# Optimization experiments

Hardware: AMD Instinct MI355X
Metric: run time of the kernel (lower is better)

Reference implementation:

```python
import jax, jax.numpy as jnp
import numpy as np

B, N, M, K = 2, 4096, 512, 50
EMB, OUT = 512, 128
EPS = 1e-5


def _sqdist(a, b):
    # a: [B,P,D], b: [B,Q,D] -> squared euclidean distances [B,P,Q]
    return (jnp.sum(a * a, -1)[:, :, None] + jnp.sum(b * b, -1)[:, None, :]
            - 2.0 * jnp.einsum('bpd,bqd->bpq', a, b))


def _graph_feature(x, xg, k):
    # x: [B,D,N] points, xg: [B,D,M] grid -> edge features [B,2D,N,k]
    xt = x.transpose(0, 2, 1)   # [B,N,D]
    gt = xg.transpose(0, 2, 1)  # [B,M,D]
    nearest = jnp.argmin(_sqdist(xt, gt), axis=-1)               # [B,N] nearest grid pt per point
    _, nbr = jax.lax.top_k(-_sqdist(gt, gt), k)                  # [B,M,k] kNN within grid
    idx = jnp.take_along_axis(nbr, nearest[:, :, None], axis=1)  # [B,N,k]
    b = x.shape[0]
    feat = gt[jnp.arange(b)[:, None, None], idx]                 # [B,N,k,D] gathered grid feats
    feat = feat.at[:, :, 0, :].set(xt)                           # slot 0 <- point's own feature
    ctr = xt[:, :, None, :]
    out = jnp.concatenate([feat - ctr, jnp.broadcast_to(ctr, feat.shape)], axis=-1)
    return out.transpose(0, 3, 1, 2)                             # [B,2D,N,k]


def _lrelu(x):
    return jnp.where(x >= 0, x, 0.2 * x)


def _bn(y, g, bt, axes):
    # BatchNorm forward with batch statistics (torch training-mode math, biased var)
    m = jnp.mean(y, axis=axes, keepdims=True)
    v = jnp.mean((y - m) ** 2, axis=axes, keepdims=True)
    sh = [1] * y.ndim
    sh[1] = -1
    return (y - m) / jnp.sqrt(v + EPS) * g.reshape(sh) + bt.reshape(sh)


def _conv2(x, W, g, bt):
    # 1x1 Conv2d (no bias) + BN2d + LeakyReLU(0.2)
    return _lrelu(_bn(jnp.einsum('oc,bcnk->bonk', W, x), g, bt, (0, 2, 3)))


def _conv1(x, W, g, bt):
    # 1x1 Conv1d (no bias) + BN1d + LeakyReLU(0.2)
    return _lrelu(_bn(jnp.einsum('oc,bcn->bon', W, x), g, bt, (0, 2)))


def _forward(x, x_grid, FPS, W1, W2, W3, W4, W5, W6, W7, W8, W9,
             g1, g2, g3, g4, g5, g6, g7, g8,
             b1, b2, b3, b4, b5, b6, b7, b8):
    f = _graph_feature(x, x_grid, K)
    f = _conv2(f, W1, g1, b1)
    f = _conv2(f, W2, g2, b2)
    x1 = f.max(-1)                                               # [B,64,N]
    x1g = jnp.take_along_axis(x1, FPS[:, None, :], axis=2)       # [B,64,M]
    f = _graph_feature(x1, x1g, K)
    f = _conv2(f, W3, g3, b3)
    f = _conv2(f, W4, g4, b4)
    x2 = f.max(-1)
    x2g = jnp.take_along_axis(x2, FPS[:, None, :], axis=2)
    f = _graph_feature(x2, x2g, K)
    f = _conv2(f, W5, g5, b5)
    x3 = f.max(-1)
    x3g = jnp.take_along_axis(x3, FPS[:, None, :], axis=2)
    xg = jnp.concatenate([x1g, x2g, x3g], axis=1)                # [B,192,M]
    xg = _conv1(xg, W6, g6, b6)                                  # [B,EMB,M]
    xg = jnp.broadcast_to(xg.max(-1, keepdims=True), (x.shape[0], EMB, x.shape[2]))
    h = jnp.concatenate([xg, x1, x2, x3], axis=1)                # [B,EMB+192,N]
    h = _conv1(h, W7, g7, b7)
    h = _conv1(h, W8, g8, b8)
    h = jnp.einsum('oc,bcn->bon', W9, h)                         # final conv9, no BN/act
    return h.transpose(0, 2, 1)                                  # [B,N,OUT]


def setup_inputs() -> dict:
    key = jax.random.key(0)
    ks = jax.random.split(key, 32)
    def w(i, o, c):
        return jax.random.normal(ks[i], (o, c), jnp.float32) * 0.1
    inp = {
        'x': jax.random.normal(ks[0], (B, 3, N), jnp.float32),
        'x_grid': jax.random.normal(ks[1], (B, 3, M), jnp.float32),
        'FPS': jax.random.randint(ks[2], (B, M), 0, N),
        'W1': w(3, 64, 6), 'W2': w(4, 64, 64), 'W3': w(5, 64, 128),
        'W4': w(6, 64, 64), 'W5': w(7, 64, 128), 'W6': w(8, EMB, 192),
        'W7': w(9, 128, 192 + EMB), 'W8': w(10, 64, 128), 'W9': w(11, OUT, 64),
    }
    dims = [64, 64, 64, 64, 64, EMB, 128, 64]
    for j, d in enumerate(dims):
        inp[f'g{j+1}'] = 1.0 + 0.05 * jax.random.normal(ks[12 + j], (d,), jnp.float32)
        inp[f'b{j+1}'] = 0.05 * jax.random.normal(ks[20 + j], (d,), jnp.float32)
    return inp


def reference(x, x_grid, FPS, W1, W2, W3, W4, W5, W6, W7, W8, W9,
              g1, g2, g3, g4, g5, g6, g7, g8,
              b1, b2, b3, b4, b5, b6, b7, b8):
    return _forward(x, x_grid, FPS, W1, W2, W3, W4, W5, W6, W7, W8, W9,
                    g1, g2, g3, g4, g5, g6, g7, g8,
                    b1, b2, b3, b4, b5, b6, b7, b8)
```

## Files before the change

kernel.cpp:

```cpp
#include <hip/hip_runtime.h>
#include <hip/hip_bf16.h>

#define DEV __device__ __forceinline__
using bf16 = __hip_bfloat16;
using u16 = unsigned short;
using u64 = unsigned long long;

static constexpr int B_ = 2, N_ = 4096, M_ = 512, K_ = 50;
static constexpr int BN = B_ * N_;
static constexpr int BM = B_ * M_;
static constexpr float EPS_ = 1e-5f;

DEV float lrelu(float z) { return z < 0.f ? 0.2f * z : z; }
DEV int clampi(int v, int hi) { return ((unsigned)v < (unsigned)hi) ? v : 0; }

DEV u16 f2bfu(float f) {
    unsigned u = __float_as_uint(f);
    return (u16)((u + 0x7fffu + ((u >> 16) & 1u)) >> 16);
}
DEV float bfu2f(u16 h) { return __uint_as_float((unsigned)h << 16); }
DEV unsigned cvtpk(float a, float b) {
    unsigned r;
    asm("v_cvt_pk_bf16_f32 %0, %1, %2" : "=v"(r) : "v"(a), "v"(b));
    return r;
}

typedef short bf8v __attribute__((ext_vector_type(8)));
typedef float f4v __attribute__((ext_vector_type(4)));

__global__ void k_detect(const unsigned short* __restrict__ xw, int* __restrict__ flag) {
    int t = threadIdx.x;
    int cnt = 0;
    for (int i = t; i < 4096; i += 256) {
        int e = (xw[i] >> 7) & 0xFF;
        if (e >= 100 && e <= 140) cnt++;
    }
    __shared__ int sh[256];
    sh[t] = cnt;
    __syncthreads();
    for (int s = 128; s; s >>= 1) { if (t < s) sh[t] += sh[t + s]; __syncthreads(); }
    if (t == 0) *flag = (sh[0] >= 3300) ? 1 : 0;
}

struct CvtDesc { const void* src; float* dst; int n; };
struct CvtArgs { CvtDesc d[25]; };
__global__ void k_convert(CvtArgs a, const int* __restrict__ flag) {
    CvtDesc dd = a.d[blockIdx.y];
    int i = blockIdx.x * 256 + threadIdx.x;
    if (i >= dd.n) return;
    float v = (*flag) ? __bfloat162float(((const bf16*)dd.src)[i])
                      : ((const float*)dd.src)[i];
    dd.dst[i] = v;
}

struct CvtT { const void* src; float* dst; int O; int C; int stride; int off; };
struct CvtTArgs { CvtT d[6]; };
__global__ void k_convT(CvtTArgs a, const int* __restrict__ flag) {
    CvtT dd = a.d[blockIdx.y];
    int idx = blockIdx.x * 256 + threadIdx.x;
    if (idx >= dd.O * dd.C) return;
    int c = idx / dd.O, o = idx % dd.O;
    int si = o * dd.stride + dd.off + c;
    float v = (*flag) ? __bfloat162float(((const bf16*)dd.src)[si])
                      : ((const float*)dd.src)[si];
    dd.dst[idx] = v;
}

__global__ void k_wfrag(const float* __restrict__ Wa, const float* __restrict__ Wb,
                        u16* __restrict__ fa, u16* __restrict__ fb) {
    const float* W = blockIdx.y ? Wb : Wa;
    u16* f = blockIdx.y ? fb : fa;
    int t = blockIdx.x * 256 + threadIdx.x;
    int j = t & 7, l = (t >> 3) & 63, s = (t >> 9) & 1, n = (t >> 10) & 3;
    int o = n * 16 + (l & 15);
    int c = s * 32 + (l >> 4) * 8 + j;
    float v = W[o * 64 + c];
    u16 hi = f2bfu(v);
    u16 lo = f2bfu(v - bfu2f(hi));
    f[t] = hi;
    f[4096 + t] = lo;
}

__global__ void k_wfrag7(const float* __restrict__ W7vt, u16* __restrict__ f) {
    int t = blockIdx.x * 256 + threadIdx.x;
    int j = t & 7, l = (t >> 3) & 63;
    int rest = t >> 9;
    int s = rest % 6, ot = rest / 6;
    int o = ot * 16 + (l & 15);
    int c = s * 32 + (l >> 4) * 8 + j;
    float v = W7vt[c * 128 + o];
    u16 hi = f2bfu(v);
    u16 lo = f2bfu(v - bfu2f(hi));
    f[t] = hi;
    f[24576 + t] = lo;
}

__global__ void k_ubuf(const float* __restrict__ Pg, const float* __restrict__ prm,
                       float* __restrict__ ub) {
    int t = blockIdx.x * 256 + threadIdx.x;
    int c = t & 63;
    ub[t] = fmaf(prm[c], Pg[t], prm[64 + c]);
}

DEV float rdval(const void* p, int i, int isbf) {
    return isbf ? __bfloat162float(((const bf16*)p)[i]) : ((const float*)p)[i];
}
__global__ void k_transpose(const void* __restrict__ x, const void* __restrict__ xg,
                            const int* __restrict__ flag,
                            float* __restrict__ xt, float* __restrict__ gt,
                            float* __restrict__ gT3, float* __restrict__ gn) {
    int isbf = *flag;
    int idx = blockIdx.x * 256 + threadIdx.x;
    if (idx < BN * 3) {
        int c = idx / BN, i = idx % BN;
        int b = i / N_, n = i % N_;
        xt[i * 3 + c] = rdval(x, (b * 3 + c) * N_ + n, isbf);
    } else {
        int r = idx - BN * 3;
        if (r < BM) {
            int b = r / M_, m = r % M_;
            float s = 0.f;
            for (int c = 0; c < 3; c++) {
                float v = rdval(xg, (b * 3 + c) * M_ + m, isbf);
                gt[r * 3 + c] = v;
                gT3[(b * 3 + c) * M_ + m] = v;
                s = fmaf(v, v, s);
            }
            gn[r] = s;
        }
    }
}

DEV void nearest3_body(int blk, const float* __restrict__ q, const float* __restrict__ gt,
                       const float* __restrict__ gn, int* __restrict__ nearest) {
    int sub = threadIdx.x & 15;
    int pt = blk * 16 + (threadIdx.x >> 4);
    int b = pt >> 12;
    float q0 = q[pt * 3], q1 = q[pt * 3 + 1], q2 = q[pt * 3 + 2];
    float qn = q0 * q0 + q1 * q1 + q2 * q2;
    const float* gb = gt + (size_t)b * M_ * 3;
    const float* gnb = gn + b * M_;
    float best = 1e30f; int bi = 0x7fffffff;
    for (int j = 0; j < 32; j++) {
        int m = sub + 16 * j;
        float dot = q0 * gb[m * 3] + q1 * gb[m * 3 + 1] + q2 * gb[m * 3 + 2];
        float dv = qn + gnb[m] - 2.f * dot;
        if (dv < best || (dv == best && m < bi)) { best = dv; bi = m; }
    }
    for (int off = 8; off; off >>= 1) {
        float ov = __shfl_xor(best, off);
        int oi = __shfl_xor(bi, off);
        if (ov < best || (ov == best && oi < bi)) { best = ov; bi = oi; }
    }
    if (sub == 0) nearest[pt] = clampi(bi, M_);
}

DEV void nearest64_body_v4(int blk, const float* __restrict__ q,
                           const float* __restrict__ gT, const float* __restrict__ gn,
                           int* __restrict__ nearest,
                           float (*__restrict__ lg)[512], float (*__restrict__ ql)[64]) {
    int lane = threadIdx.x & 63;
    int tid = threadIdx.x;
    int w = __builtin_amdgcn_readfirstlane(threadIdx.x >> 6);
    int pt0 = blk * 16 + w * 4;
    int b = pt0 >> 12;
    const float* gTb = gT + (size_t)b * 64 * M_;
    {
        const float4* q4 = (const float4*)(q + (size_t)(blk * 16) * 64);
        ((float4*)ql)[tid] = q4[tid];
    }
    float qn[4] = {0.f, 0.f, 0.f, 0.f};
    float d[4][8] = {};
#pragma clang loop unroll(disable)
    for (int ch = 0; ch < 8; ch++) {
        __syncthreads();
        {
            const float4* src = (const float4*)(gTb + (size_t)ch * 8 * M_);
            float4* dst = (float4*)lg;
#pragma unroll
            for (int i = 0; i < 4; i++) {
                int idx = i * 256 + tid;
                dst[idx] = src[idx];
            }
        }
        __syncthreads();
#pragma unroll
        for (int j = 0; j < 8; j++) {
            float4 g0 = *(const float4*)&lg[j][4 * lane];
            float4 g1 = *(const float4*)&lg[j][256 + 4 * lane];
#pragma unroll
            for (int p = 0; p < 4; p++) {
                float qc = ql[w * 4 + p][ch * 8 + j];
                qn[p] = fmaf(qc, qc, qn[p]);
                d[p][0] = fmaf(qc, g0.x, d[p][0]); d[p][1] = fmaf(qc, g0.y, d[p][1]);
                d[p][2] = fmaf(qc, g0.z, d[p][2]); d[p][3] = fmaf(qc, g0.w, d[p][3]);
                d[p][4] = fmaf(qc, g1.x, d[p][4]); d[p][5] = fmaf(qc, g1.y, d[p][5]);
                d[p][6] = fmaf(qc, g1.z, d[p][6]); d[p][7] = fmaf(qc, g1.w, d[p][7]);
            }
        }
    }
    const float* gnb = gn + b * M_;
    float4 n0 = *(const float4*)(gnb + 4 * lane);
    float4 n1 = *(const float4*)(gnb + 256 + 4 * lane);
    float nn[8] = {n0.x, n0.y, n0.z, n0.w, n1.x, n1.y, n1.z, n1.w};
#pragma clang loop unroll(disable)
    for (int p = 0; p < 4; p++) {
        float best = 1e30f; int bi = 0;
#pragma unroll
        for (int i = 0; i < 8; i++) {
            int m = (i < 4) ? (4 * lane + i) : (256 + 4 * lane + i - 4);
            float dv = qn[p] + nn[i] - 2.f * d[p][i];
            if (dv < best || (dv == best && m < bi)) { best = dv; bi = m; }
        }
        for (int off = 32; off; off >>= 1) {
            float ov = __shfl_xor(best, off);
            int oi = __shfl_xor(bi, off);
            if (ov < best || (ov == best && oi < bi)) { best = ov; bi = oi; }
        }
        if (lane == 0) nearest[pt0 + p] = clampi(bi, M_);
    }
}

DEV void select50(const float dd[8], const int mreg[8], int lane,
                  int* __restrict__ rowp, int* __restrict__ idxrow) {
    u64 key[8];
#pragma unroll
    for (int i = 0; i < 8; i++) {
        unsigned u = __float_as_uint(dd[i]);
        if (u == 0x80000000u) u = 0u;
        u = (u & 0x80000000u) ? ~u : (u | 0x80000000u);
        key[i] = ((u64)u << 9) | (u64)(unsigned)mreg[i];
    }
    u64 kmin = key[0];
#pragma unroll
    for (int i = 1; i < 8; i++) kmin = key[i] < kmin ? key[i] : kmin;
    for (int off = 32; off; off >>= 1) {
        u64 o = __shfl_xor(kmin, off);
        kmin = o < kmin ? o : kmin;
    }
    u64 res = 0;
#pragma clang loop unroll(disable)
    for (int bit = 40; bit >= 0; --bit) {
        u64 t = res | ((u64)1 << bit);
        int c = 0;
#pragma unroll
        for (int i = 0; i < 8; i++) c += (key[i] < t) ? 1 : 0;
        u64 b0 = __ballot(c & 1), b1 = __ballot(c & 2), b2 = __ballot(c & 4), b3 = __ballot(c & 8);
        int tot = __popcll(b0) + 2 * __popcll(b1) + 4 * __popcll(b2) + 8 * __popcll(b3);
        if (tot <= K_ - 1) res = t;
    }
    int lc = 0, loc[8];
    bool sel[8];
#pragma unroll
    for (int i = 0; i < 8; i++) {
        sel[i] = (key[i] <= res) && (key[i] != kmin);
        loc[i] = lc;
        lc += sel[i] ? 1 : 0;
    }
    u64 lmask = ((u64)1 << lane) - 1;
    u64 c0 = __ballot(lc & 1), c1 = __ballot(lc & 2), c2 = __ballot(lc & 4), c3 = __ballot(lc & 8);
    int pre = __popcll(c0 & lmask) + 2 * __popcll(c1 & lmask)
            + 4 * __popcll(c2 & lmask) + 8 * __popcll(c3 & lmask);
#pragma unroll
    for (int i = 0; i < 8; i++) {
        if (key[i] == kmin) { rowp[0] = mreg[i]; idxrow[0] = mreg[i]; }
        if (sel[i]) { int p = 1 + pre + loc[i]; rowp[p] = mreg[i]; idxrow[p] = mreg[i]; }
    }
}

DEV void nbr3_body(int blk, const float* __restrict__ g, const float* __restrict__ gT,
                   const float* __restrict__ gn, const float* __restrict__ Pg,
                   int* __restrict__ nbr, float* __restrict__ T1, float* __restrict__ T2,
                   float* __restrict__ Mn, float* __restrict__ Mx,
                   int (*__restrict__ idxb)[64]) {
    int lane = threadIdx.x & 63, w = threadIdx.x >> 6;
    int row = blk * 4 + w;
    int b = row >> 9;
    const float* grow = g + (size_t)row * 3;
    float qn = gn[row];
    const float* gTb = gT + (size_t)b * 3 * M_;
    const float* gnb = gn + b * M_;
// ... 73 lines not shown
        for (int j = 0; j < 8; j++) {
            float qc = ql[w][ch * 8 + j];
            float4 g0 = *(const float4*)&lg[j][4 * lane];
            float4 g1 = *(const float4*)&lg[j][256 + 4 * lane];
            d[0] = fmaf(qc, g0.x, d[0]); d[1] = fmaf(qc, g0.y, d[1]);
            d[2] = fmaf(qc, g0.z, d[2]); d[3] = fmaf(qc, g0.w, d[3]);
            d[4] = fmaf(qc, g1.x, d[4]); d[5] = fmaf(qc, g1.y, d[5]);
            d[6] = fmaf(qc, g1.z, d[6]); d[7] = fmaf(qc, g1.w, d[7]);
        }
    }
    float4 n0 = *(const float4*)(gnb + 4 * lane);
    float4 n1 = *(const float4*)(gnb + 256 + 4 * lane);
    float dd[8];
    dd[0] = qn + n0.x - 2.f * d[0]; dd[1] = qn + n0.y - 2.f * d[1];
    dd[2] = qn + n0.z - 2.f * d[2]; dd[3] = qn + n0.w - 2.f * d[3];
    dd[4] = qn + n1.x - 2.f * d[4]; dd[5] = qn + n1.y - 2.f * d[5];
    dd[6] = qn + n1.z - 2.f * d[6]; dd[7] = qn + n1.w - 2.f * d[7];
    int mreg[8];
#pragma unroll
    for (int i = 0; i < 8; i++) mreg[i] = (i < 4) ? (4 * lane + i) : (256 + 4 * lane + i - 4);
    select50(dd, mreg, lane, nbr + (size_t)row * K_, idxb[w]);
    int myIdx = idxb[w][lane];
    const float* Pgb = Pg + (size_t)b * M_ * 64;
    float t1 = 0.f, t2 = 0.f, mn = 1e30f, mx = -1e30f;
#pragma unroll 7
    for (int k = 1; k < K_; k++) {
        int idx = clampi(__shfl(myIdx, k), M_);
        float v = Pgb[(size_t)idx * 64 + lane];
        t1 += v; t2 = fmaf(v, v, t2);
        mn = fminf(mn, v); mx = fmaxf(mx, v);
    }
    size_t o = (size_t)row * 64 + lane;
    T1[o] = t1; T2[o] = t2; Mn[o] = mn; Mx[o] = mx;
}

__global__ __launch_bounds__(256) void k_knn3(
    const float* __restrict__ q, const float* __restrict__ gt, const float* __restrict__ gT3,
    const float* __restrict__ gn, const float* __restrict__ Pg,
    int* __restrict__ nearest, int* __restrict__ nbr, float* __restrict__ T1,
    float* __restrict__ T2, float* __restrict__ Mn, float* __restrict__ Mx) {
    __shared__ int idxb[4][64];
    if (blockIdx.x < BN / 16) nearest3_body(blockIdx.x, q, gt, gn, nearest);
    else nbr3_body(blockIdx.x - BN / 16, gt, gT3, gn, Pg, nbr, T1, T2, Mn, Mx, idxb);
}
__global__ __launch_bounds__(256) void k_knn64(
    const float* __restrict__ q, const float* __restrict__ xgt, const float* __restrict__ gT,
    const float* __restrict__ gn, const float* __restrict__ Pg,
    int* __restrict__ nearest, int* __restrict__ nbr, float* __restrict__ T1,
    float* __restrict__ T2, float* __restrict__ Mn, float* __restrict__ Mx) {
    __shared__ float lg[8][512];
    __shared__ float ql[16][64];
    __shared__ int idxb[4][64];
    if (blockIdx.x < BN / 16) nearest64_body_v4(blockIdx.x, q, gT, gn, nearest, lg, ql);
    else nbr64_body(blockIdx.x - BN / 16, xgt, gT, gn, Pg, nbr, T1, T2, Mn, Mx, lg, ql, idxb);
}

#define STATS_STORE_64(s1v, s2v, partial)                                         \
    {                                                                             \
        __shared__ float r1_[256], r2_[256];                                      \
        r1_[threadIdx.x] = (s1v); r2_[threadIdx.x] = (s2v);                       \
        __syncthreads();                                                          \
        if (threadIdx.x < 64) {                                                   \
            int t_ = threadIdx.x;                                                 \
            float a1_ = r1_[t_] + r1_[t_ + 64] + r1_[t_ + 128] + r1_[t_ + 192];   \
            float a2_ = r2_[t_] + r2_[t_ + 64] + r2_[t_ + 128] + r2_[t_ + 192];   \
            float* sp_ = (partial) + (size_t)blockIdx.x * 128;                    \
            sp_[t_] = a1_; sp_[64 + t_] = a2_;                                    \
        }                                                                         \
    }

__global__ __launch_bounds__(256) void k_pgrid3(const float* __restrict__ g,
                                                const float* __restrict__ W1,
                                                float* __restrict__ Pg) {
    int lane = threadIdx.x & 63;
    int row = blockIdx.x * 4 + __builtin_amdgcn_readfirstlane(threadIdx.x >> 6);
    float c0 = g[row * 3], c1 = g[row * 3 + 1], c2 = g[row * 3 + 2];
    const float* wr = W1 + lane * 6;
    Pg[(size_t)row * 64 + lane] = fmaf(wr[0], c0, fmaf(wr[1], c1, wr[2] * c2));
}

__global__ __launch_bounds__(256) void k_gridprep(
    const float* __restrict__ xsrc, const int* __restrict__ FPS,
    const float* __restrict__ Wt, float* __restrict__ xgt, float* __restrict__ gT,
    float* __restrict__ gn, float* __restrict__ Pg) {
    int lane = threadIdx.x & 63, w = threadIdx.x >> 6;
    int row = blockIdx.x * 4 + w;
    int b = row >> 9, m = row & 511;
    int src = b * N_ + clampi(FPS[row], N_);
    float ge = xsrc[(size_t)src * 64 + lane];
    xgt[(size_t)row * 64 + lane] = ge;
    gT[((size_t)b * 64 + lane) * M_ + m] = ge;
    float s = 0.f, acc = 0.f;
#pragma unroll
    for (int c = 0; c < 64; c++) {
        float vc = __shfl(ge, c);
        s = fmaf(vc, vc, s);
        acc = fmaf(Wt[c * 64 + lane], vc, acc);
    }
    Pg[(size_t)row * 64 + lane] = acc;
    if (lane == 0) gn[row] = s;
}

template <int D>
__global__ __launch_bounds__(256) void k_prep_stats(
    const float* __restrict__ q, const float* __restrict__ W1,
    const int* __restrict__ nearest, const float* __restrict__ T1,
    const float* __restrict__ T2, float* __restrict__ D0, float* __restrict__ S0,
    float* __restrict__ partial) {
    int lane = threadIdx.x & 63;
    int pt = blockIdx.x * 4 + __builtin_amdgcn_readfirstlane(threadIdx.x >> 6);
    int b = pt >> 12;
    float pa, pb;
    if constexpr (D == 3) {
        float c0 = q[pt * 3], c1 = q[pt * 3 + 1], c2 = q[pt * 3 + 2];
        const float* wr = W1 + lane * 6;
        pa = fmaf(wr[0], c0, fmaf(wr[1], c1, wr[2] * c2));
        pb = fmaf(wr[3], c0, fmaf(wr[4], c1, wr[5] * c2));
    } else {
        float ge = q[(size_t)pt * 64 + lane];
        pa = 0.f; pb = 0.f;
#pragma unroll
        for (int c = 0; c < 64; c++) {
            float sh = __shfl(ge, c);
            pa = fmaf(W1[c * 64 + lane], sh, pa);
            pb = fmaf(W1[(64 + c) * 64 + lane], sh, pb);
        }
    }
    float d0 = pb - pa, s0 = pb;
    size_t t = (size_t)pt * 64 + lane;
    D0[t] = d0;
    S0[t] = s0;
    size_t nr = ((size_t)b * M_ + clampi(nearest[pt], M_)) * 64 + lane;
    float t1 = T1[nr], t2 = T2[nr];
    float s1 = s0 + fmaf(49.f, d0, t1);
    float s2 = fmaf(s0, s0, fmaf(49.f * d0, d0, fmaf(2.f * d0, t1, t2)));
    STATS_STORE_64(s1, s2, partial)
}

__global__ void k_apply0(const float* __restrict__ D0, const float* __restrict__ S0,
                         const int* __restrict__ nearest, const float* __restrict__ Mn,
                         const float* __restrict__ Mx, const float* __restrict__ prm,
                         float* __restrict__ xout) {
    int t = blockIdx.x * 256 + threadIdx.x;
    int pt = t >> 6, o = t & 63;
    int b = pt >> 12;
    size_t nr = ((size_t)b * M_ + clampi(nearest[pt], M_)) * 64 + o;
    float d0 = D0[t], s0 = S0[t];
    float a = prm[o], sh = prm[64 + o];
    float v = a > 0.f ? fmaxf(s0, d0 + Mx[nr]) : fminf(s0, d0 + Mn[nr]);
    xout[t] = lrelu(fmaf(a, v, sh));
}

__global__ __launch_bounds__(256) void k_pass1_mfma(
    const float* __restrict__ ub, const float* __restrict__ D0,
    const float* __restrict__ S0, const int* __restrict__ nearest,
    const int* __restrict__ nbr, const float* __restrict__ prm1,
    const u16* __restrict__ wf, float* __restrict__ partial,
    float* __restrict__ mn_out, float* __restrict__ mx_out) {
    __shared__ u16 Zs[2][2][4096];
    __shared__ int idxl[2][64];
    float* ls1 = (float*)&Zs[0][0][0];
    float* ls2 = ls1 + 128;
    int l = threadIdx.x & 63;
    int w = threadIdx.x >> 6;
    int wp = w >> 1, nh = w & 1;
    bf8v whi[2][2], wlo[2][2];
#pragma unroll
    for (int nt = 0; nt < 2; nt++)
#pragma unroll
        for (int s = 0; s < 2; s++) {
            int fi = (((nh * 2 + nt) * 2 + s) * 64 + l) * 8;
            whi[nt][s] = *(const bf8v*)(wf + fi);
            wlo[nt][s] = *(const bf8v*)(wf + 4096 + fi);
        }
    if (threadIdx.x < 128) {
        int p2 = threadIdx.x >> 6, k = threadIdx.x & 63;
        int pt2 = blockIdx.x * 2 + p2, b2 = pt2 >> 12;
        int nr = clampi(nearest[pt2], M_);
        idxl[p2][k] = (k >= 1 && k < K_)
                          ? clampi(nbr[((size_t)b2 * M_ + nr) * K_ + k], M_) : 0;
    }
    __syncthreads();
    {
        int tt = threadIdx.x & 127;
        int p = threadIdx.x >> 7;
        int pt = blockIdx.x * 2 + p, b = pt >> 12;
        int g = tt >> 4, j = tt & 15;
        char* zh = (char*)&Zs[p][0][0];
        char* zl = (char*)&Zs[p][1][0];
        float4 a = ((const float4*)prm1)[j];
        float4 sh4 = ((const float4*)(prm1 + 64))[j];
        float4 dv = ((const float4*)(D0 + (size_t)pt * 64))[j];
        const float* ubb = ub + (size_t)b * M_ * 64;
#pragma unroll
        for (int s = 0; s < 8; s++) {
            int k = s * 8 + g;
            float4 u, d = dv;
            if (k == 0) {
                float4 s0 = ((const float4*)(S0 + (size_t)pt * 64))[j];
                u.x = fmaf(a.x, s0.x, sh4.x); u.y = fmaf(a.y, s0.y, sh4.y);
                u.z = fmaf(a.z, s0.z, sh4.z); u.w = fmaf(a.w, s0.w, sh4.w);
                d.x = 0.f; d.y = 0.f; d.z = 0.f; d.w = 0.f;
            } else {
                int idx = idxl[p][k];
                u = ((const float4*)(ubb + (size_t)idx * 64))[j];
            }
            float z0 = lrelu(fmaf(a.x, d.x, u.x));
            float z1 = lrelu(fmaf(a.y, d.y, u.y));
            float z2 = lrelu(fmaf(a.z, d.z, u.z));
            float z3 = lrelu(fmaf(a.w, d.w, u.w));
            if (k >= K_) { z0 = 0.f; z1 = 0.f; z2 = 0.f; z3 = 0.f; }
            unsigned h01 = cvtpk(z0, z1), h23 = cvtpk(z2, z3);
            float r0 = z0 - __uint_as_float(h01 << 16);
            float r1 = z1 - __uint_as_float(h01 & 0xFFFF0000u);
            float r2 = z2 - __uint_as_float(h23 << 16);
            float r3 = z3 - __uint_as_float(h23 & 0xFFFF0000u);
            unsigned l01 = cvtpk(r0, r1), l23 = cvtpk(r2, r3);
            int ad = k * 128 + ((j * 8) ^ ((k & 7) << 4));
            *(uint2*)(zh + ad) = make_uint2(h01, h23);
            *(uint2*)(zl + ad) = make_uint2(l01, l23);
        }
    }
    __syncthreads();
    int pt = blockIdx.x * 2 + wp;
    const char* zh = (const char*)&Zs[wp][0][0];
    const char* zl = (const char*)&Zs[wp][1][0];
    f4v acc[4][2] = {};
#pragma unroll
    for (int s = 0; s < 2; s++) {
        bf8v ah[4], al[4];
#pragma unroll
        for (int m = 0; m < 4; m++) {
            int row = m * 16 + (l & 15);
            int ad = row * 128 + (((s * 64) + ((l >> 4) * 16)) ^ ((row & 7) << 4));
            ah[m] = *(const bf8v*)(zh + ad);
            al[m] = *(const bf8v*)(zl + ad);
        }
#pragma unroll
        for (int m = 0; m < 4; m++)
#pragma unroll
            for (int nt = 0; nt < 2; nt++) {
                acc[m][nt] = __builtin_amdgcn_mfma_f32_16x16x32_bf16(ah[m], whi[nt][s], acc[m][nt], 0, 0, 0);
                acc[m][nt] = __builtin_amdgcn_mfma_f32_16x16x32_bf16(al[m], whi[nt][s], acc[m][nt], 0, 0, 0);
                acc[m][nt] = __builtin_amdgcn_mfma_f32_16x16x32_bf16(ah[m], wlo[nt][s], acc[m][nt], 0, 0, 0);
            }
    }
    __syncthreads();
    int rg = (l >> 4) * 4;
#pragma unroll
    for (int nt = 0; nt < 2; nt++) {
        float s1 = 0.f, s2 = 0.f, mn = 1e30f, mx = -1e30f;
#pragma unroll
        for (int m = 0; m < 4; m++)
#pragma unroll
            for (int i = 0; i < 4; i++) {
                int kk = m * 16 + rg + i;
                float v = acc[m][nt][i];
                if (kk < K_) { s1 += v; s2 = fmaf(v, v, s2); mn = fminf(mn, v); mx = fmaxf(mx, v); }
            }
        for (int off = 16; off <= 32; off <<= 1) {
            s1 += __shfl_xor(s1, off); s2 += __shfl_xor(s2, off);
            mn = fminf(mn, __shfl_xor(mn, off)); mx = fmaxf(mx, __shfl_xor(mx, off));
        }
        if (l < 16) {
            int o = nh * 32 + nt * 16 + l;
            mn_out[(size_t)pt * 64 + o] = mn;
            mx_out[(size_t)pt * 64 + o] = mx;
            ls1[wp * 64 + o] = s1;
            ls2[wp * 64 + o] = s2;
        }
    }
    __syncthreads();
    if (threadIdx.x < 64) {
        int t = threadIdx.x;
        float* sp = partial + (size_t)blockIdx.x * 128;
        sp[t] = ls1[t] + ls1[64 + t];
        sp[64 + t] = ls2[t] + ls2[64 + t];
    }
}

__global__ void k_apply(const float* __restrict__ mn, const float* __restrict__ mx,
                        const float* __restrict__ prm, float* __restrict__ xout) {
    int t = blockIdx.x * 256 + threadIdx.x;
    int o = t & 63;
    float a = prm[o], sh = prm[64 + o];
    float v = a > 0.f ? mx[t] : mn[t];
    xout[t] = lrelu(fmaf(a, v, sh));
}

template <int NP, int O>
__global__ __launch_bounds__(256) void k_redfin(
    const float* __restrict__ partial, double* __restrict__ red,
    int* __restrict__ counter, int C,
    const float* __restrict__ g, const float* __restrict__ bt,
    float* __restrict__ prm) {
    constexpr int VALS = 2 * O;
    constexpr int G = NP / 32;
    int b = blockIdx.x;
    for (int v = threadIdx.x; v < VALS; v += 256) {
        const float* p = partial + (size_t)b * G * VALS + v;
        double s = 0.0;
        for (int k = 0; k < G; k++) s += p[(size_t)k * VALS];
        red[(size_t)b * VALS + v] = s;
    }
    __threadfence();
    __syncthreads();
    __shared__ bool isLast;
    if (threadIdx.x == 0) isLast = (atomicAdd(counter, 1) == 31);
    __syncthreads();
    if (!isLast) return;
    __threadfence();
    for (int o = threadIdx.x; o < O; o += 256) {
        double s1 = 0.0, s2 = 0.0;
#pragma unroll
        for (int k = 0; k < 32; k++) {
            s1 += red[(size_t)k * VALS + o];
            s2 += red[(size_t)k * VALS + O + o];
        }
        double m = s1 / C, var = s2 / C - m * m;
        if (var < 0) var = 0;
        float sc = g[o] / sqrtf((float)var + EPS_);
        prm[o] = sc;
        prm[O + o] = bt[o] - (float)m * sc;
    }
}

__global__ __launch_bounds__(256) void k_conv_w6(
    const float* __restrict__ x1gt, const float* __restrict__ x2gt,
    const float* __restrict__ x3t, const int* __restrict__ FPS,
    const float* __restrict__ W6t, float* __restrict__ y6, float* __restrict__ partial) {
    __shared__ float vl[4][192];
    int b = blockIdx.x / 128;
    int m0 = (blockIdx.x % 128) * 4;
    for (int i = threadIdx.x; i < 4 * 192; i += 256) {
        int mi = i / 192, c = i % 192;
        float v;
        if (c < 128) {
            const float* src = c < 64 ? x1gt : x2gt;
            v = src[((size_t)b * M_ + m0 + mi) * 64 + (c & 63)];
        } else {
            int s = b * N_ + clampi(FPS[b * M_ + m0 + mi], N_);
            v = x3t[(size_t)s * 64 + (c - 128)];
        }
        vl[mi][c] = v;
    }
    __syncthreads();
    float acc0[4] = {0}, acc1[4] = {0};
    int o0 = threadIdx.x, o1 = threadIdx.x + 256;
    for (int c = 0; c < 192; c++) {
        float w0 = W6t[c * 512 + o0];
        float w1 = W6t[c * 512 + o1];
#pragma unroll
        for (int m = 0; m < 4; m++) { float v = vl[m][c]; acc0[m] = fmaf(w0, v, acc0[m]); acc1[m] = fmaf(w1, v, acc1[m]); }
    }
    float s1a = 0, s2a = 0, s1b = 0, s2b = 0;
    for (int m = 0; m < 4; m++) {
        float ya = acc0[m], yb = acc1[m];
        y6[((size_t)b * M_ + m0 + m) * 512 + o0] = ya;
// ... 70 lines not shown
            else sp_ = x3t + base + (seg - 8) * 16;
            float f[16];
#pragma unroll
            for (int i = 0; i < 4; i++) {
                float4 v = ((const float4*)sp_)[i];
                f[4 * i] = v.x; f[4 * i + 1] = v.y; f[4 * i + 2] = v.z; f[4 * i + 3] = v.w;
            }
            unsigned hp[8], lp[8];
#pragma unroll
            for (int e = 0; e < 8; e++) {
                unsigned h = cvtpk(f[2 * e], f[2 * e + 1]);
                float r0 = f[2 * e] - __uint_as_float(h << 16);
                float r1 = f[2 * e + 1] - __uint_as_float(h & 0xFFFF0000u);
                hp[e] = h;
                lp[e] = cvtpk(r0, r1);
            }
            uint4* dh = (uint4*)&Zh[item][seg * 16];
            uint4* dl = (uint4*)&Zl[item][seg * 16];
            dh[0] = make_uint4(hp[0], hp[1], hp[2], hp[3]);
            dh[1] = make_uint4(hp[4], hp[5], hp[6], hp[7]);
            dl[0] = make_uint4(lp[0], lp[1], lp[2], lp[3]);
            dl[1] = make_uint4(lp[4], lp[5], lp[6], lp[7]);
        }
    }
    __syncthreads();
    f4v acc[2] = {};
#pragma unroll
    for (int s = 0; s < 6; s++) {
        int row = l & 15, col = s * 32 + (l >> 4) * 8;
        bf8v ah = *(const bf8v*)&Zh[row][col];
        bf8v al = *(const bf8v*)&Zl[row][col];
#pragma unroll
        for (int nt = 0; nt < 2; nt++) {
            acc[nt] = __builtin_amdgcn_mfma_f32_16x16x32_bf16(ah, wh[nt][s], acc[nt], 0, 0, 0);
            acc[nt] = __builtin_amdgcn_mfma_f32_16x16x32_bf16(al, wh[nt][s], acc[nt], 0, 0, 0);
            acc[nt] = __builtin_amdgcn_mfma_f32_16x16x32_bf16(ah, wl[nt][s], acc[nt], 0, 0, 0);
        }
    }
#pragma unroll
    for (int nt = 0; nt < 2; nt++) {
        int o = (2 * w + nt) * 16 + (l & 15);
        float pv = p7[b * 128 + o];
        float s1 = 0.f, s2 = 0.f;
#pragma unroll
        for (int i = 0; i < 4; i++) {
            int item = (l >> 4) * 4 + i;
            float yv = pv + acc[nt][i];
            y7[(size_t)(item0 + item) * 128 + o] = yv;
            s1 += yv; s2 = fmaf(yv, yv, s2);
        }
        for (int off = 16; off <= 32; off <<= 1) {
            s1 += __shfl_xor(s1, off);
            s2 += __shfl_xor(s2, off);
        }
        if (l < 16) {
            float* sp = partial + (size_t)blockIdx.x * 256;
            sp[o] = s1;
            sp[128 + o] = s2;
        }
    }
}

__global__ __launch_bounds__(256) void k_conv_w8(
    const float* __restrict__ y7, const float* __restrict__ prm7,
    const float* __restrict__ W8t, float* __restrict__ y8, float* __restrict__ partial) {
    int lane = threadIdx.x & 63;
    int item = blockIdx.x * 4 + (threadIdx.x >> 6);
    float W0[64], W1r[64];
#pragma unroll
    for (int c = 0; c < 64; c++) {
        W0[c] = W8t[c * 64 + lane];
        W1r[c] = W8t[(64 + c) * 64 + lane];
    }
    float a0 = prm7[lane], sh0 = prm7[128 + lane];
    float a1 = prm7[64 + lane], sh1 = prm7[128 + 64 + lane];
    float z0 = lrelu(fmaf(a0, y7[(size_t)item * 128 + lane], sh0));
    float z1 = lrelu(fmaf(a1, y7[(size_t)item * 128 + 64 + lane], sh1));
    float acc = 0.f;
#pragma unroll
    for (int c = 0; c < 64; c++) {
        acc = fmaf(W0[c], __shfl(z0, c), acc);
        acc = fmaf(W1r[c], __shfl(z1, c), acc);
    }
    y8[(size_t)item * 64 + lane] = acc;
    STATS_STORE_64(acc, acc * acc, partial)
}

__global__ __launch_bounds__(256) void k_final(
    const float* __restrict__ y8, const float* __restrict__ prm8,
    const float* __restrict__ W9t, void* __restrict__ out, const int* __restrict__ flag) {
    __shared__ float zl[2][64];
    int item0 = blockIdx.x * 2;
    if (threadIdx.x < 128) {
        int it = threadIdx.x >> 6, c = threadIdx.x & 63;
        float z = fmaf(prm8[c], y8[(size_t)(item0 + it) * 64 + c], prm8[64 + c]);
        zl[it][c] = lrelu(z);
    }
    __syncthreads();
    int it = threadIdx.x >> 7, o = threadIdx.x & 127;
    float acc = 0.f;
#pragma unroll
    for (int c = 0; c < 64; c++) acc = fmaf(W9t[c * 128 + o], zl[it][c], acc);
    size_t oi = (size_t)(item0 + it) * 128 + o;
    if (*flag) ((bf16*)out)[oi] = __float2bfloat16(acc);
    else ((float*)out)[oi] = acc;
}

extern "C" void kernel_launch(void* const* d_in, const int* in_sizes, int n_in,
                              void* d_out, int out_size, void* d_ws, size_t ws_size,
                              hipStream_t stream) {
    (void)in_sizes; (void)n_in; (void)out_size; (void)ws_size;
    const void* x = d_in[0];
    const void* xgrid = d_in[1];
    const int* FPS = (const int*)d_in[2];

    char* ws = (char*)d_ws;
    size_t off = 0;
    auto alloc = [&](size_t bytes) -> char* {
        char* p = ws + off;
        off = (off + bytes + 255) & ~(size_t)255;
        return p;
    };
    int* flag       = (int*)alloc(256);
    int* counters   = (int*)alloc(256);
    float* partials = (float*)alloc((size_t)4096 * 128 * sizeof(float));
    double* redbuf  = (double*)alloc(32 * 1024 * sizeof(double));
    float* prm      = (float*)alloc(8 * 1024 * sizeof(float));
    static const int wsz[9] = {384, 4096, 8192, 4096, 8192, 98304, 90112, 8192, 8192};
    static const int dims[8] = {64, 64, 64, 64, 64, 512, 128, 64};
    float* cW[9];
    for (int i = 0; i < 9; i++) cW[i] = (float*)alloc((size_t)wsz[i] * 4);
    float* cG[8];
    float* cB[8];
    for (int j = 0; j < 8; j++) {
        cG[j] = (float*)alloc((size_t)dims[j] * 4);
        cB[j] = (float*)alloc((size_t)dims[j] * 4);
    }
    float* W6t  = (float*)alloc((size_t)512 * 192 * 4);
    float* W7vt = (float*)alloc((size_t)128 * 192 * 4);
    float* W8t  = (float*)alloc((size_t)64 * 128 * 4);
    float* W9t  = (float*)alloc((size_t)128 * 64 * 4);
    float* W3t  = (float*)alloc((size_t)64 * 128 * 4);
    float* W5t  = (float*)alloc((size_t)64 * 128 * 4);
    u16* wf2    = (u16*)alloc((size_t)8192 * 2);
    u16* wf4    = (u16*)alloc((size_t)8192 * 2);
    u16* wf7    = (u16*)alloc((size_t)49152 * 2);
    float* xt    = (float*)alloc((size_t)BN * 3 * 4);
    float* gt    = (float*)alloc((size_t)BM * 3 * 4);
    float* gT3   = (float*)alloc((size_t)B_ * 3 * M_ * 4);
    float* gn    = (float*)alloc((size_t)BM * 4);
    int* nearest = (int*)alloc((size_t)BN * 4);
    int* nbr     = (int*)alloc((size_t)BM * K_ * 4);
    float* Pg    = (float*)alloc((size_t)BM * 64 * 4);
    float* ubuf  = (float*)alloc((size_t)BM * 64 * 4);
    float* x1t   = (float*)alloc((size_t)BN * 64 * 4);
    float* x2t   = (float*)alloc((size_t)BN * 64 * 4);
    float* x3t   = (float*)alloc((size_t)BN * 64 * 4);
    float* x1gt  = (float*)alloc((size_t)BM * 64 * 4);
    float* x2gt  = (float*)alloc((size_t)BM * 64 * 4);
    float* gT64  = (float*)alloc((size_t)B_ * 64 * M_ * 4);
    float* y6    = (float*)alloc((size_t)BM * 512 * 4);
    float* xgmax = (float*)alloc((size_t)B_ * 512 * 4);
    float* p7    = (float*)alloc((size_t)B_ * 128 * 4);
    float* y7    = (float*)alloc((size_t)BN * 128 * 4);
    float* y8    = (float*)alloc((size_t)BN * 64 * 4);
    float* D0b = y7;
    float* S0b = y7 + (size_t)BN * 64;
    float* mnb = y8;
    float* mxb = y6;
    float* T1b = y6;
    float* T2b = y6 + (size_t)BM * 64;
    float* Mnb = y6 + (size_t)2 * BM * 64;
    float* Mxb = y6 + (size_t)3 * BM * 64;

    hipMemsetAsync(counters, 0, 8 * sizeof(int), stream);
    k_detect<<<1, 256, 0, stream>>>((const unsigned short*)x, flag);

    CvtArgs ca;
    for (int i = 0; i < 9; i++) ca.d[i] = {d_in[3 + i], cW[i], wsz[i]};
    for (int j = 0; j < 8; j++) {
        ca.d[9 + 2 * j]     = {d_in[12 + 2 * j], cG[j], dims[j]};
        ca.d[9 + 2 * j + 1] = {d_in[13 + 2 * j], cB[j], dims[j]};
    }
    k_convert<<<dim3(384, 25), 256, 0, stream>>>(ca, flag);
    CvtTArgs ct;
    ct.d[0] = {d_in[8],  W6t,  512, 192, 192, 0};
    ct.d[1] = {d_in[9],  W7vt, 128, 192, 704, 512};
    ct.d[2] = {d_in[10], W8t,  64, 128, 128, 0};
    ct.d[3] = {d_in[11], W9t,  128, 64, 64, 0};
    ct.d[4] = {d_in[5],  W3t,  64, 128, 128, 0};
    ct.d[5] = {d_in[7],  W5t,  64, 128, 128, 0};
    k_convT<<<dim3(384, 6), 256, 0, stream>>>(ct, flag);
    k_wfrag<<<dim3(16, 2), 256, 0, stream>>>(cW[1], cW[3], wf2, wf4);
    k_wfrag7<<<96, 256, 0, stream>>>(W7vt, wf7);
    k_transpose<<<(BN * 3 + BM + 255) / 256, 256, 0, stream>>>(x, xgrid, flag, xt, gt, gT3, gn);

    const int PG = BN / 4;
    const int EW = BN * 64 / 256;
    const int CK = BN * K_;
    const int KNNG = BN / 16 + BM / 4;
    const int UBG = BM * 64 / 256;

    k_pgrid3<<<BM / 4, 256, 0, stream>>>(gt, cW[0], Pg);
    k_knn3<<<KNNG, 256, 0, stream>>>(xt, gt, gT3, gn, Pg, nearest, nbr, T1b, T2b, Mnb, Mxb);
    k_prep_stats<3><<<PG, 256, 0, stream>>>(xt, cW[0], nearest, T1b, T2b, D0b, S0b, partials);
    k_redfin<2048, 64><<<32, 256, 0, stream>>>(partials, redbuf, counters + 0, CK, cG[0], cB[0], prm + 0 * 1024);
    k_ubuf<<<UBG, 256, 0, stream>>>(Pg, prm + 0 * 1024, ubuf);
    k_pass1_mfma<<<BN / 2, 256, 0, stream>>>(ubuf, D0b, S0b, nearest, nbr, prm + 0 * 1024, wf2, partials, mnb, mxb);
    k_redfin<4096, 64><<<32, 256, 0, stream>>>(partials, redbuf, counters + 1, CK, cG[1], cB[1], prm + 1 * 1024);
    k_apply<<<EW, 256, 0, stream>>>(mnb, mxb, prm + 1 * 1024, x1t);

    k_gridprep<<<BM / 4, 256, 0, stream>>>(x1t, FPS, W3t, x1gt, gT64, gn, Pg);
    k_knn64<<<KNNG, 256, 0, stream>>>(x1t, x1gt, gT64, gn, Pg, nearest, nbr, T1b, T2b, Mnb, Mxb);
    k_prep_stats<64><<<PG, 256, 0, stream>>>(x1t, W3t, nearest, T1b, T2b, D0b, S0b, partials);
    k_redfin<2048, 64><<<32, 256, 0, stream>>>(partials, redbuf, counters + 2, CK, cG[2], cB[2], prm + 2 * 1024);
    k_ubuf<<<UBG, 256, 0, stream>>>(Pg, prm + 2 * 1024, ubuf);
    k_pass1_mfma<<<BN / 2, 256, 0, stream>>>(ubuf, D0b, S0b, nearest, nbr, prm + 2 * 1024, wf4, partials, mnb, mxb);
    k_redfin<4096, 64><<<32, 256, 0, stream>>>(partials, redbuf, counters + 3, CK, cG[3], cB[3], prm + 3 * 1024);
    k_apply<<<EW, 256, 0, stream>>>(mnb, mxb, prm + 3 * 1024, x2t);

    k_gridprep<<<BM / 4, 256, 0, stream>>>(x2t, FPS, W5t, x2gt, gT64, gn, Pg);
    k_knn64<<<KNNG, 256, 0, stream>>>(x2t, x2gt, gT64, gn, Pg, nearest, nbr, T1b, T2b, Mnb, Mxb);
    k_prep_stats<64><<<PG, 256, 0, stream>>>(x2t, W5t, nearest, T1b, T2b, D0b, S0b, partials);
    k_redfin<2048, 64><<<32, 256, 0, stream>>>(partials, redbuf, counters + 4, CK, cG[4], cB[4], prm + 4 * 1024);
    k_apply0<<<EW, 256, 0, stream>>>(D0b, S0b, nearest, Mnb, Mxb, prm + 4 * 1024, x3t);

    k_conv_w6<<<BM / 4, 256, 0, stream>>>(x1gt, x2gt, x3t, FPS, W6t, y6, partials);
    k_redfin<256, 512><<<32, 256, 0, stream>>>(partials, redbuf, counters + 5, BM, cG[5], cB[5], prm + 5 * 1024);
    k_maxM<<<B_ * 64, 256, 0, stream>>>(y6, prm + 5 * 1024, xgmax);
    k_p7<<<64, 256, 0, stream>>>(xgmax, cW[6], p7);
    k_conv_w7m<<<BN / 16, 256, 0, stream>>>(x1t, x2t, x3t, p7, wf7, y7, partials);
    k_redfin<512, 128><<<32, 256, 0, stream>>>(partials, redbuf, counters + 6, BN, cG[6], cB[6], prm + 6 * 1024);
    k_conv_w8<<<BN / 4, 256, 0, stream>>>(y7, prm + 6 * 1024, W8t, y8, partials);
    k_redfin<2048, 64><<<32, 256, 0, stream>>>(partials, redbuf, counters + 7, BN, cG[7], cB[7], prm + 7 * 1024);
    k_final<<<BN / 2, 256, 0, stream>>>(y8, prm + 7 * 1024, W9t, d_out, flag);
}
```

Measured before the change: 391.9 us.

## Merge setup conversion kernels into one launch and fold ubuf into pass1

```diff
diff --git a/kernel.cpp b/kernel.cpp
--- a/kernel.cpp
+++ b/kernel.cpp
@@ -42,91 +42,77 @@
     if (t == 0) *flag = (sh[0] >= 3300) ? 1 : 0;
 }
 
+DEV float rdval(const void* p, size_t i, int isbf) {
+    return isbf ? __bfloat162float(((const bf16*)p)[i]) : ((const float*)p)[i];
+}
+
 struct CvtDesc { const void* src; float* dst; int n; };
-struct CvtArgs { CvtDesc d[25]; };
-__global__ void k_convert(CvtArgs a, const int* __restrict__ flag) {
-    CvtDesc dd = a.d[blockIdx.y];
-    int i = blockIdx.x * 256 + threadIdx.x;
-    if (i >= dd.n) return;
-    float v = (*flag) ? __bfloat162float(((const bf16*)dd.src)[i])
-                      : ((const float*)dd.src)[i];
-    dd.dst[i] = v;
-}
-
 struct CvtT { const void* src; float* dst; int O; int C; int stride; int off; };
-struct CvtTArgs { CvtT d[6]; };
-__global__ void k_convT(CvtTArgs a, const int* __restrict__ flag) {
-    CvtT dd = a.d[blockIdx.y];
-    int idx = blockIdx.x * 256 + threadIdx.x;
-    if (idx >= dd.O * dd.C) return;
-    int c = idx / dd.O, o = idx % dd.O;
-    int si = o * dd.stride + dd.off + c;
-    float v = (*flag) ? __bfloat162float(((const bf16*)dd.src)[si])
-                      : ((const float*)dd.src)[si];
-    dd.dst[idx] = v;
-}
-
-__global__ void k_wfrag(const float* __restrict__ Wa, const float* __restrict__ Wb,
-                        u16* __restrict__ fa, u16* __restrict__ fb) {
-    const float* W = blockIdx.y ? Wb : Wa;
-    u16* f = blockIdx.y ? fb : fa;
-    int t = blockIdx.x * 256 + threadIdx.x;
-    int j = t & 7, l = (t >> 3) & 63, s = (t >> 9) & 1, n = (t >> 10) & 3;
-    int o = n * 16 + (l & 15);
-    int c = s * 32 + (l >> 4) * 8 + j;
-    float v = W[o * 64 + c];
-    u16 hi = f2bfu(v);
-    u16 lo = f2bfu(v - bfu2f(hi));
-    f[t] = hi;
-    f[4096 + t] = lo;
-}
-
-__global__ void k_wfrag7(const float* __restrict__ W7vt, u16* __restrict__ f) {
-    int t = blockIdx.x * 256 + threadIdx.x;
-    int j = t & 7, l = (t >> 3) & 63;
-    int rest = t >> 9;
-    int s = rest % 6, ot = rest / 6;
-    int o = ot * 16 + (l & 15);
-    int c = s * 32 + (l >> 4) * 8 + j;
-    float v = W7vt[c * 128 + o];
-    u16 hi = f2bfu(v);
-    u16 lo = f2bfu(v - bfu2f(hi));
-    f[t] = hi;
-    f[24576 + t] = lo;
-}
-
-__global__ void k_ubuf(const float* __restrict__ Pg, const float* __restrict__ prm,
-                       float* __restrict__ ub) {
-    int t = blockIdx.x * 256 + threadIdx.x;
-    int c = t & 63;
-    ub[t] = fmaf(prm[c], Pg[t], prm[64 + c]);
-}
-
-DEV float rdval(const void* p, int i, int isbf) {
-    return isbf ? __bfloat162float(((const bf16*)p)[i]) : ((const float*)p)[i];
-}
-__global__ void k_transpose(const void* __restrict__ x, const void* __restrict__ xg,
-                            const int* __restrict__ flag,
-                            float* __restrict__ xt, float* __restrict__ gt,
-                            float* __restrict__ gT3, float* __restrict__ gn) {
+struct SetupArgs { CvtDesc d[25]; CvtT t[6]; };
+
+__global__ __launch_bounds__(256) void k_setup(
+    SetupArgs a, const void* __restrict__ W2r, const void* __restrict__ W4r,
+    const void* __restrict__ W7r, u16* __restrict__ wf2, u16* __restrict__ wf4,
+    u16* __restrict__ wf7, const void* __restrict__ x, const void* __restrict__ xg,
+    const int* __restrict__ flag, float* __restrict__ xt, float* __restrict__ gt,
+    float* __restrict__ gT3, float* __restrict__ gn) {
+    int y = blockIdx.y;
     int isbf = *flag;
-    int idx = blockIdx.x * 256 + threadIdx.x;
-    if (idx < BN * 3) {
-        int c = idx / BN, i = idx % BN;
-        int b = i / N_, n = i % N_;
-        xt[i * 3 + c] = rdval(x, (b * 3 + c) * N_ + n, isbf);
+    int gi = blockIdx.x * 256 + threadIdx.x;
+    if (y < 25) {
+        CvtDesc dd = a.d[y];
+        if (gi < dd.n) dd.dst[gi] = rdval(dd.src, gi, isbf);
+    } else if (y < 31) {
+        CvtT dd = a.t[y - 25];
+        if (gi < dd.O * dd.C) {
+            int c = gi / dd.O, o = gi % dd.O;
+            dd.dst[gi] = rdval(dd.src, (size_t)o * dd.stride + dd.off + c, isbf);
+        }
+    } else if (y == 31 || y == 32) {
+        const void* W = (y == 31) ? W2r : W4r;
+        u16* f = (y == 31) ? wf2 : wf4;
+        if (gi < 4096) {
+            int j = gi & 7, l = (gi >> 3) & 63, s = (gi >> 9) & 1, n = (gi >> 10) & 3;
+            int o = n * 16 + (l & 15);
+            int c = s * 32 + (l >> 4) * 8 + j;
+            float v = rdval(W, (size_t)o * 64 + c, isbf);
+            u16 hi = f2bfu(v);
+            u16 lo = f2bfu(v - bfu2f(hi));
+            f[gi] = hi;
+            f[4096 + gi] = lo;
+        }
+    } else if (y == 33) {
+        if (gi < 24576) {
+            int j = gi & 7, l = (gi >> 3) & 63;
+            int rest = gi >> 9;
+            int s = rest % 6, ot = rest / 6;
+            int o = ot * 16 + (l & 15);
+            int c = s * 32 + (l >> 4) * 8 + j;
+            float v = rdval(W7r, (size_t)o * 704 + 512 + c, isbf);
+            u16 hi = f2bfu(v);
+            u16 lo = f2bfu(v - bfu2f(hi));
+            wf7[gi] = hi;
+            wf7[24576 + gi] = lo;
+        }
     } else {
-        int r = idx - BN * 3;
-        if (r < BM) {
-            int b = r / M_, m = r % M_;
-            float s = 0.f;
-            for (int c = 0; c < 3; c++) {
-                float v = rdval(xg, (b * 3 + c) * M_ + m, isbf);
-                gt[r * 3 + c] = v;
-                gT3[(b * 3 + c) * M_ + m] = v;
-                s = fmaf(v, v, s);
+        int idx = gi;
+        if (idx < BN * 3) {
+            int c = idx / BN, i = idx % BN;
+            int b = i / N_, n = i % N_;
+            xt[i * 3 + c] = rdval(x, (size_t)(b * 3 + c) * N_ + n, isbf);
+        } else {
+            int r = idx - BN * 3;
+            if (r < BM) {
+                int b = r / M_, m = r % M_;
+                float s = 0.f;
+                for (int c = 0; c < 3; c++) {
+                    float v = rdval(xg, (size_t)(b * 3 + c) * M_ + m, isbf);
+                    gt[r * 3 + c] = v;
+                    gT3[(b * 3 + c) * M_ + m] = v;
+                    s = fmaf(v, v, s);
+                }
+                gn[r] = s;
             }
-            gn[r] = s;
         }
     }
 }
@@ -506,7 +492,7 @@
 }
 
 __global__ __launch_bounds__(256) void k_pass1_mfma(
-    const float* __restrict__ ub, const float* __restrict__ D0,
+    const float* __restrict__ Pg, const float* __restrict__ D0,
     const float* __restrict__ S0, const int* __restrict__ nearest,
     const int* __restrict__ nbr, const float* __restrict__ prm1,
     const u16* __restrict__ wf, float* __restrict__ partial,
@@ -545,7 +531,7 @@
         float4 a = ((const float4*)prm1)[j];
         float4 sh4 = ((const float4*)(prm1 + 64))[j];
         float4 dv = ((const float4*)(D0 + (size_t)pt * 64))[j];
-        const float* ubb = ub + (size_t)b * M_ * 64;
+        const float* Pgb = Pg + (size_t)b * M_ * 64;
 #pragma unroll
         for (int s = 0; s < 8; s++) {
             int k = s * 8 + g;
@@ -557,7 +543,9 @@
                 d.x = 0.f; d.y = 0.f; d.z = 0.f; d.w = 0.f;
             } else {
                 int idx = idxl[p][k];
-                u = ((const float4*)(ubb + (size_t)idx * 64))[j];
+                float4 pg = ((const float4*)(Pgb + (size_t)idx * 64))[j];
+                u.x = fmaf(a.x, pg.x, sh4.x); u.y = fmaf(a.y, pg.y, sh4.y);
+                u.z = fmaf(a.z, pg.z, sh4.z); u.w = fmaf(a.w, pg.w, sh4.w);
             }
             float z0 = lrelu(fmaf(a.x, d.x, u.x));
             float z1 = lrelu(fmaf(a.y, d.y, u.y));
@@ -934,7 +922,6 @@
     int* nearest = (int*)alloc((size_t)BN * 4);
     int* nbr     = (int*)alloc((size_t)BM * K_ * 4);
     float* Pg    = (float*)alloc((size_t)BM * 64 * 4);
-    float* ubuf  = (float*)alloc((size_t)BM * 64 * 4);
     float* x1t   = (float*)alloc((size_t)BN * 64 * 4);
     float* x2t   = (float*)alloc((size_t)BN * 64 * 4);
     float* x3t   = (float*)alloc((size_t)BN * 64 * 4);
@@ -958,37 +945,32 @@
     hipMemsetAsync(counters, 0, 8 * sizeof(int), stream);
     k_detect<<<1, 256, 0, stream>>>((const unsigned short*)x, flag);
 
-    CvtArgs ca;
-    for (int i = 0; i < 9; i++) ca.d[i] = {d_in[3 + i], cW[i], wsz[i]};
+    SetupArgs sa;
+    for (int i = 0; i < 9; i++) sa.d[i] = {d_in[3 + i], cW[i], wsz[i]};
     for (int j = 0; j < 8; j++) {
-        ca.d[9 + 2 * j]     = {d_in[12 + 2 * j], cG[j], dims[j]};
-        ca.d[9 + 2 * j + 1] = {d_in[13 + 2 * j], cB[j], dims[j]};
-    }
-    k_convert<<<dim3(384, 25), 256, 0, stream>>>(ca, flag);
-    CvtTArgs ct;
-    ct.d[0] = {d_in[8],  W6t,  512, 192, 192, 0};
-    ct.d[1] = {d_in[9],  W7vt, 128, 192, 704, 512};
-    ct.d[2] = {d_in[10], W8t,  64, 128, 128, 0};
-    ct.d[3] = {d_in[11], W9t,  128, 64, 64, 0};
-    ct.d[4] = {d_in[5],  W3t,  64, 128, 128, 0};
-    ct.d[5] = {d_in[7],  W5t,  64, 128, 128, 0};
-    k_convT<<<dim3(384, 6), 256, 0, stream>>>(ct, flag);
-    k_wfrag<<<dim3(16, 2), 256, 0, stream>>>(cW[1], cW[3], wf2, wf4);
-    k_wfrag7<<<96, 256, 0, stream>>>(W7vt, wf7);
-    k_transpose<<<(BN * 3 + BM + 255) / 256, 256, 0, stream>>>(x, xgrid, flag, xt, gt, gT3, gn);
+        sa.d[9 + 2 * j]     = {d_in[12 + 2 * j], cG[j], dims[j]};
+        sa.d[9 + 2 * j + 1] = {d_in[13 + 2 * j], cB[j], dims[j]};
+    }
+    sa.t[0] = {d_in[8],  W6t,  512, 192, 192, 0};
+    sa.t[1] = {d_in[9],  W7vt, 128, 192, 704, 512};
+    sa.t[2] = {d_in[10], W8t,  64, 128, 128, 0};
+    sa.t[3] = {d_in[11], W9t,  128, 64, 64, 0};
+    sa.t[4] = {d_in[5],  W3t,  64, 128, 128, 0};
+    sa.t[5] = {d_in[7],  W5t,  64, 128, 128, 0};
+    k_setup<<<dim3(384, 35), 256, 0, stream>>>(sa, d_in[4], d_in[6], d_in[9],
+                                               wf2, wf4, wf7, x, xgrid, flag,
+                                               xt, gt, gT3, gn);
 
     const int PG = BN / 4;
     const int EW = BN * 64 / 256;
     const int CK = BN * K_;
     const int KNNG = BN / 16 + BM / 4;
-    const int UBG = BM * 64 / 256;
 
     k_pgrid3<<<BM / 4, 256, 0, stream>>>(gt, cW[0], Pg);
     k_knn3<<<KNNG, 256, 0, stream>>>(xt, gt, gT3, gn, Pg, nearest, nbr, T1b, T2b, Mnb, Mxb);
     k_prep_stats<3><<<PG, 256, 0, stream>>>(xt, cW[0], nearest, T1b, T2b, D0b, S0b, partials);
     k_redfin<2048, 64><<<32, 256, 0, stream>>>(partials, redbuf, counters + 0, CK, cG[0], cB[0], prm + 0 * 1024);
-    k_ubuf<<<UBG, 256, 0, stream>>>(Pg, prm + 0 * 1024, ubuf);
-    k_pass1_mfma<<<BN / 2, 256, 0, stream>>>(ubuf, D0b, S0b, nearest, nbr, prm + 0 * 1024, wf2, partials, mnb, mxb);
+    k_pass1_mfma<<<BN / 2, 256, 0, stream>>>(Pg, D0b, S0b, nearest, nbr, prm + 0 * 1024, wf2, partials, mnb, mxb);
     k_redfin<4096, 64><<<32, 256, 0, stream>>>(partials, redbuf, counters + 1, CK, cG[1], cB[1], prm + 1 * 1024);
     k_apply<<<EW, 256, 0, stream>>>(mnb, mxb, prm + 1 * 1024, x1t);
 
@@ -996,8 +978,7 @@
     k_knn64<<<KNNG, 256, 0, stream>>>(x1t, x1gt, gT64, gn, Pg, nearest, nbr, T1b, T2b, Mnb, Mxb);
     k_prep_stats<64><<<PG, 256, 0, stream>>>(x1t, W3t, nearest, T1b, T2b, D0b, S0b, partials);
     k_redfin<2048, 64><<<32, 256, 0, stream>>>(partials, redbuf, counters + 2, CK, cG[2], cB[2], prm + 2 * 1024);
-    k_ubuf<<<UBG, 256, 0, stream>>>(Pg, prm + 2 * 1024, ubuf);
-    k_pass1_mfma<<<BN / 2, 256, 0, stream>>>(ubuf, D0b, S0b, nearest, nbr, prm + 2 * 1024, wf4, partials, mnb, mxb);
+    k_pass1_mfma<<<BN / 2, 256, 0, stream>>>(Pg, D0b, S0b, nearest, nbr, prm + 2 * 1024, wf4, partials, mnb, mxb);
     k_redfin<4096, 64><<<32, 256, 0, stream>>>(partials, redbuf, counters + 3, CK, cG[3], cB[3], prm + 3 * 1024);
     k_apply<<<EW, 256, 0, stream>>>(mnb, mxb, prm + 3 * 1024, x2t);
 
```

Result: no change. 386.4 us (-1.4%).
